# Kernel optimization log

Hardware: AMD Instinct MI355X
Metric: run time of the kernel (lower is better)

The kernel has to match this reference:

```python
import jax, jax.numpy as jnp
import numpy as np

N, E, B, D = 50000, 800000, 250, 128
EPS = 1e-5


def setup_inputs() -> dict:
    key = jax.random.key(0)
    ks = jax.random.split(key, 12)
    x = jax.random.normal(ks[0], (N, D), jnp.float32)
    w = jax.random.uniform(ks[1], (E, 4), jnp.float32)
    src = jax.random.randint(ks[2], (E,), 0, N)
    dst = jax.random.randint(ks[3], (E,), 0, N)
    graph_ids = jnp.sort(jax.random.randint(ks[4], (N,), 0, B))
    s = 1.0 / np.sqrt(D)
    W1 = jax.random.normal(ks[5], (D, D), jnp.float32) * s
    W2 = jax.random.normal(ks[6], (D, D), jnp.float32) * s
    W3 = jax.random.normal(ks[7], (D, D), jnp.float32) * s
    ln1_g = jnp.ones((D,), jnp.float32)
    ln1_b = jnp.zeros((D,), jnp.float32)
    ln2_g = jnp.ones((D,), jnp.float32)
    ln2_b = jnp.zeros((D,), jnp.float32)
    return dict(x=x, w=w, W1=W1, W2=W2, W3=W3, ln1_g=ln1_g, ln1_b=ln1_b,
                ln2_g=ln2_g, ln2_b=ln2_b, src=src, dst=dst, graph_ids=graph_ids)


def _layernorm(h, g, b):
    mu = jnp.mean(h, axis=-1, keepdims=True)
    var = jnp.mean(jnp.square(h - mu), axis=-1, keepdims=True)
    return (h - mu) * jax.lax.rsqrt(var + EPS) * g + b


def reference(x, w, W1, W2, W3, ln1_g, ln1_b, ln2_g, ln2_b, src, dst, graph_ids):
    # edge feature [E,Fe] -> scalar edge weight [E] (mean over feature dim)
    w_s = jnp.mean(w, axis=-1)
    ones_e = jnp.ones((E,), x.dtype)
    # DGL norm='both': unweighted degrees, clamped to >= 1
    out_deg = jnp.clip(jax.ops.segment_sum(ones_e, src, num_segments=N), 1.0)
    in_deg = jnp.clip(jax.ops.segment_sum(ones_e, dst, num_segments=N), 1.0)
    out_norm = jax.lax.rsqrt(out_deg)[:, None]  # [N,1]
    in_norm = jax.lax.rsqrt(in_deg)[:, None]    # [N,1]

    def gconv(h, W):
        m = (h * out_norm)[src] * w_s[:, None]                 # [E,D] gather-mul
        agg = jax.ops.segment_sum(m, dst, num_segments=N)      # [N,D] scatter-add
        return (agg * in_norm) @ W                              # [N,D_out]

    h = _layernorm(jax.nn.relu(gconv(x, W1)), ln1_g, ln1_b)
    h = _layernorm(jax.nn.relu(gconv(h, W2)), ln2_g, ln2_b)
    h = gconv(h, W3)
    # per-graph segmented sum readout -> [B, D]
    return jax.ops.segment_sum(h, graph_ids, num_segments=B)
```

## Files before the change

kernel.cpp:

```cpp
#include <hip/hip_runtime.h>

#define D 128
#define RS 16
#define NBMAX 1024
constexpr float EPS = 1e-5f;

typedef short bf16x8 __attribute__((ext_vector_type(8)));
typedef float f32x4 __attribute__((ext_vector_type(4)));
typedef unsigned long long u64;

__device__ __forceinline__ uint f2bf(float f) {
  union { float f; uint u; } v; v.f = f;
  return (v.u + 0x7fffu + ((v.u >> 16) & 1u)) >> 16;
}
__device__ __forceinline__ float bflo(uint u) {
  union { uint u; float f; } v; v.u = u << 16; return v.f;
}
__device__ __forceinline__ float bfhi(uint u) {
  union { uint u; float f; } v; v.u = u & 0xffff0000u; return v.f;
}

__device__ __forceinline__ int lower_bound(const int* __restrict__ a, int n, int key) {
  int lo = 0, hi = n;
  while (lo < hi) { int m = (lo + hi) >> 1; if (a[m] < key) lo = m + 1; else hi = m; }
  return lo;
}

__global__ __launch_bounds__(256) void k_pre(
    const int* __restrict__ src, const int* __restrict__ dst,
    int* __restrict__ ocnt, int* __restrict__ btot, int E, int nb, int ebA,
    const float4* __restrict__ x, uint4* __restrict__ xb, int n8, int cb,
    const float* __restrict__ W1, const float* __restrict__ W2,
    const float* __restrict__ W3, ushort* __restrict__ Wf) {
  __shared__ int hloc[NBMAX];
  int bid = blockIdx.x;
  int tid = threadIdx.x;
  if (bid < ebA) {
    for (int j = tid; j < nb; j += 256) hloc[j] = 0;
    __syncthreads();
    int e0 = bid * 4096;
#pragma unroll 4
    for (int it = 0; it < 16; ++it) {
      int e = e0 + it * 256 + tid;
      if (e < E) {
        atomicAdd(&ocnt[src[e]], 1);
        atomicAdd(&hloc[dst[e] >> 6], 1);
      }
    }
    __syncthreads();
    for (int j = tid; j < nb; j += 256) {
      int c = hloc[j];
      if (c) atomicAdd(&btot[j], c);
    }
  } else if (bid < ebA + cb) {
    int i = (bid - ebA) * 256 + tid;
    if (i < n8) {
      float4 p = x[i * 2], q = x[i * 2 + 1];
      uint4 o;
      o.x = f2bf(p.x) | (f2bf(p.y) << 16);
      o.y = f2bf(p.z) | (f2bf(p.w) << 16);
      o.z = f2bf(q.x) | (f2bf(q.y) << 16);
      o.w = f2bf(q.z) | (f2bf(q.w) << 16);
      xb[i] = o;
    }
  } else {
    int t4 = (bid - ebA - cb) * 256 + tid;
    if (t4 < 3 * 2048) {
      const float* Wsrc = (t4 < 2048) ? W1 : (t4 < 4096) ? W2 : W3;
      int t = t4 & 2047;
      int lane = t & 63;
      int frag = t >> 6;
      int ks = frag >> 3, ct = frag & 7;
      int col = ct * 16 + (lane & 15);
      int kb = ks * 32 + (lane >> 4) * 8;
      uint p[8];
#pragma unroll
      for (int j = 0; j < 8; ++j) p[j] = f2bf(Wsrc[(kb + j) * D + col]);
      uint4 o;
      o.x = p[0] | (p[1] << 16);
      o.y = p[2] | (p[3] << 16);
      o.z = p[4] | (p[5] << 16);
      o.w = p[6] | (p[7] << 16);
      *(uint4*)(Wf + (size_t)t4 * 8) = o;
    }
  }
}

__global__ void k_onorm(const int* __restrict__ ocnt, float* __restrict__ outn, int N) {
  int n = blockIdx.x * 256 + threadIdx.x;
  if (n < N) outn[n] = rsqrtf(fmaxf((float)ocnt[n], 1.0f));
}

__global__ __launch_bounds__(1024) void k_bbase(const int* __restrict__ btot,
                                                int* __restrict__ bb,
                                                int* __restrict__ rowptr,
                                                int nb, int E, int N) {
  __shared__ int part[1024];
  int t = threadIdx.x;
  int v = (t < nb) ? btot[t] : 0;
  part[t] = v;
  __syncthreads();
  for (int off = 1; off < 1024; off <<= 1) {
    int u = (t >= off) ? part[t - off] : 0;
    __syncthreads();
    part[t] += u;
    __syncthreads();
  }
  if (t < nb) bb[t] = part[t] - v;
  if (t == 0) { bb[nb] = E; rowptr[N] = E; }
}

__global__ __launch_bounds__(256) void k_bscatter(
    const int* __restrict__ src, const int* __restrict__ dst,
    const float4* __restrict__ w, const float* __restrict__ outn,
    const int* __restrict__ bb, int* __restrict__ bcur,
    u64* __restrict__ ebuf, int E, int nb) {
  __shared__ int hloc[NBMAX];
  __shared__ int hcur[NBMAX];
  int bid = blockIdx.x, tid = threadIdx.x;
  for (int j = tid; j < nb; j += 256) hloc[j] = 0;
  __syncthreads();
  int e0 = bid * 4096;
#pragma unroll 4
  for (int it = 0; it < 16; ++it) {
    int e = e0 + it * 256 + tid;
    if (e < E) atomicAdd(&hloc[dst[e] >> 6], 1);
  }
  __syncthreads();
  for (int j = tid; j < nb; j += 256) {
    int c = hloc[j];
    hcur[j] = c ? (bb[j] + atomicAdd(&bcur[j], c)) : 0;
  }
  __syncthreads();
#pragma unroll 4
  for (int it = 0; it < 16; ++it) {
    int e = e0 + it * 256 + tid;
    if (e < E) {
      int d = dst[e], s = src[e];
      int pos = atomicAdd(&hcur[d >> 6], 1);
      float4 wv = w[e];
      float coef = (wv.x + wv.y + wv.z + wv.w) * 0.25f * outn[s];
      u64 pk = ((u64)__float_as_uint(coef) << 32) |
               ((u64)(d & 63) << 16) | (uint)s;
      ebuf[pos] = pk;
    }
  }
}

__global__ __launch_bounds__(256) void k_bplace(
    const u64* __restrict__ ebuf, const int* __restrict__ bb,
    int* __restrict__ rowptr, float* __restrict__ innm,
    u64* __restrict__ ecsr, int N) {
  __shared__ int c64[64], ex[64], cur[64];
  int b = blockIdx.x, tid = threadIdx.x;
  int base = bb[b];
  int cnt = bb[b + 1] - base;
  if (tid < 64) c64[tid] = 0;
  __syncthreads();
  for (int i = tid; i < cnt; i += 256) {
    u64 v = ebuf[base + i];
    atomicAdd(&c64[(int)((v >> 16) & 63)], 1);
  }
  __syncthreads();
  if (tid < 64) {
    int cv = c64[tid];
    int inc = cv;
#pragma unroll
    for (int off = 1; off < 64; off <<= 1) {
      int u = __shfl_up(inc, off);
      if (tid >= off) inc += u;
    }
    int excl = inc - cv;
    ex[tid] = excl;
    cur[tid] = 0;
    int node = b * 64 + tid;
    if (node < N) {
      rowptr[node] = base + excl;
      innm[node] = rsqrtf(fmaxf((float)cv, 1.0f));
    }
  }
  __syncthreads();
  for (int i = tid; i < cnt; i += 256) {
    u64 v = ebuf[base + i];
    int dl = (int)((v >> 16) & 63);
    int pos = base + ex[dl] + atomicAdd(&cur[dl], 1);
    ecsr[pos] = (v & 0xFFFFFFFF00000000ull) | (v & 0xFFFFull);
  }
}

__global__ __launch_bounds__(128) void k_fused(
    const ushort* __restrict__ h, const int* __restrict__ rowptr,
    const u64* __restrict__ ecsr,
    const float* __restrict__ innm, const ushort* __restrict__ Wf,
    const float* __restrict__ g, const float* __restrict__ bta,
    void* __restrict__ out, int N, int do_ln) {
  __shared__ float lds[16 * D];
  const int lane = threadIdx.x & 63;
  const int wid = threadIdx.x >> 6;
  const int lr = lane & 15, lg = lane >> 4;
  const int row0 = blockIdx.x * 16;
  const int row = row0 + lr;
  const bool valid = row < N;

  int beg = 0, end = 0;
  float sc = 0.f;
  if (valid) { beg = rowptr[row]; end = rowptr[row + 1]; sc = innm[row]; }

  float a0[8], a1[8], a2[8], a3[8];
#pragma unroll
  for (int i = 0; i < 8; ++i) { a0[i] = 0; a1[i] = 0; a2[i] = 0; a3[i] = 0; }

#define EDGE(J)                                                  \
  {                                                              \
    u64 v = ecsr[J];                                             \
    float cf = __uint_as_float((uint)(v >> 32));                 \
    int s = (int)(v & 0xFFFFFFFFu);                              \
    const ushort* hp = h + (size_t)s * D + lg * 8;               \
    uint4 q0 = *(const uint4*)(hp);                              \
    uint4 q1 = *(const uint4*)(hp + 32);                         \
    uint4 q2 = *(const uint4*)(hp + 64);                         \
    uint4 q3 = *(const uint4*)(hp + 96);                         \
    a0[0] = fmaf(bflo(q0.x), cf, a0[0]); a0[1] = fmaf(bfhi(q0.x), cf, a0[1]); \
    a0[2] = fmaf(bflo(q0.y), cf, a0[2]); a0[3] = fmaf(bfhi(q0.y), cf, a0[3]); \
    a0[4] = fmaf(bflo(q0.z), cf, a0[4]); a0[5] = fmaf(bfhi(q0.z), cf, a0[5]); \
    a0[6] = fmaf(bflo(q0.w), cf, a0[6]); a0[7] = fmaf(bfhi(q0.w), cf, a0[7]); \
    a1[0] = fmaf(bflo(q1.x), cf, a1[0]); a1[1] = fmaf(bfhi(q1.x), cf, a1[1]); \
    a1[2] = fmaf(bflo(q1.y), cf, a1[2]); a1[3] = fmaf(bfhi(q1.y), cf, a1[3]); \
    a1[4] = fmaf(bflo(q1.z), cf, a1[4]); a1[5] = fmaf(bfhi(q1.z), cf, a1[5]); \
    a1[6] = fmaf(bflo(q1.w), cf, a1[6]); a1[7] = fmaf(bfhi(q1.w), cf, a1[7]); \
    a2[0] = fmaf(bflo(q2.x), cf, a2[0]); a2[1] = fmaf(bfhi(q2.x), cf, a2[1]); \
    a2[2] = fmaf(bflo(q2.y), cf, a2[2]); a2[3] = fmaf(bfhi(q2.y), cf, a2[3]); \
    a2[4] = fmaf(bflo(q2.z), cf, a2[4]); a2[5] = fmaf(bfhi(q2.z), cf, a2[5]); \
    a2[6] = fmaf(bflo(q2.w), cf, a2[6]); a2[7] = fmaf(bfhi(q2.w), cf, a2[7]); \
    a3[0] = fmaf(bflo(q3.x), cf, a3[0]); a3[1] = fmaf(bfhi(q3.x), cf, a3[1]); \
    a3[2] = fmaf(bflo(q3.y), cf, a3[2]); a3[3] = fmaf(bfhi(q3.y), cf, a3[3]); \
    a3[4] = fmaf(bflo(q3.z), cf, a3[4]); a3[5] = fmaf(bfhi(q3.z), cf, a3[5]); \
    a3[6] = fmaf(bflo(q3.w), cf, a3[6]); a3[7] = fmaf(bfhi(q3.w), cf, a3[7]); \
  }

  int j = beg + wid;
  for (; j + 2 < end; j += 4) { EDGE(j) EDGE(j + 2) }
  if (j < end) EDGE(j)
#undef EDGE

  if (wid == 1) {
#pragma unroll
    for (int i = 0; i < 8; ++i) {
      lds[i * 64 + lane]        = a0[i];
      lds[(i + 8) * 64 + lane]  = a1[i];
      lds[(i + 16) * 64 + lane] = a2[i];
      lds[(i + 24) * 64 + lane] = a3[i];
    }
  }
  __syncthreads();
  if (wid == 1) return;
#pragma unroll
  for (int i = 0; i < 8; ++i) {
    a0[i] += lds[i * 64 + lane];
    a1[i] += lds[(i + 8) * 64 + lane];
    a2[i] += lds[(i + 16) * 64 + lane];
    a3[i] += lds[(i + 24) * 64 + lane];
  }
  asm volatile("s_waitcnt lgkmcnt(0)" ::: "memory");
  __builtin_amdgcn_sched_barrier(0);

  uint4 fa[4];
#define PACK(dst, A)                                             \
  dst.x = f2bf(A[0] * sc) | (f2bf(A[1] * sc) << 16);             \
  dst.y = f2bf(A[2] * sc) | (f2bf(A[3] * sc) << 16);             \
  dst.z = f2bf(A[4] * sc) | (f2bf(A[5] * sc) << 16);             \
  dst.w = f2bf(A[6] * sc) | (f2bf(A[7] * sc) << 16);
  PACK(fa[0], a0) PACK(fa[1], a1) PACK(fa[2], a2) PACK(fa[3], a3)
#undef PACK

  f32x4 acc[8];
#pragma unroll
  for (int ct = 0; ct < 8; ++ct) acc[ct] = (f32x4){0.f, 0.f, 0.f, 0.f};
#pragma unroll
  for (int ks = 0; ks < 4; ++ks) {
    bf16x8 av;
    __builtin_memcpy(&av, &fa[ks], 16);
    const ushort* wp = Wf + ((size_t)(ks * 8) * 64 + lane) * 8;
#pragma unroll
    for (int ct = 0; ct < 8; ++ct) {
      bf16x8 b = *(const bf16x8*)(wp + ct * 512);
      acc[ct] = __builtin_amdgcn_mfma_f32_16x16x32_bf16(av, b, acc[ct], 0, 0, 0);
    }
  }

  if (do_ln) {
    float v[8][4];
#pragma unroll
    for (int ct = 0; ct < 8; ++ct)
#pragma unroll
      for (int j2 = 0; j2 < 4; ++j2) v[ct][j2] = fmaxf(acc[ct][j2], 0.f);
    float mu[4], rs[4];
#pragma unroll
    for (int j2 = 0; j2 < 4; ++j2) {
      float s = 0.f;
#pragma unroll
      for (int ct = 0; ct < 8; ++ct) s += v[ct][j2];
#pragma unroll
      for (int off = 1; off < 16; off <<= 1) s += __shfl_xor(s, off);
      mu[j2] = s * (1.0f / D);
    }
#pragma unroll
    for (int j2 = 0; j2 < 4; ++j2) {
      float q = 0.f;
#pragma unroll
      for (int ct = 0; ct < 8; ++ct) {
        v[ct][j2] -= mu[j2];
        q = fmaf(v[ct][j2], v[ct][j2], q);
      }
#pragma unroll
      for (int off = 1; off < 16; off <<= 1) q += __shfl_xor(q, off);
      rs[j2] = rsqrtf(q * (1.0f / D) + EPS);
    }
    ushort* lp = (ushort*)&lds[0];
#pragma unroll
    for (int ct = 0; ct < 8; ++ct) {
      float gc = g[ct * 16 + lr], bc = bta[ct * 16 + lr];
#pragma unroll
      for (int j2 = 0; j2 < 4; ++j2)
        lp[(lg * 4 + j2) * D + ct * 16 + lr] = (ushort)f2bf(fmaf(v[ct][j2] * rs[j2], gc, bc));
    }
    __builtin_amdgcn_wave_barrier();
    int r = row0 + (lane >> 2);
    if (r < N) {
      ushort* ob = (ushort*)out + (size_t)row0 * D + lane * 32;
#pragma unroll
      for (int i = 0; i < 4; ++i)
        ((uint4*)ob)[i] = ((const uint4*)(lp + lane * 32))[i];
    }
  } else {
    float* lp = &lds[0];
#pragma unroll
    for (int ct = 0; ct < 8; ++ct)
#pragma unroll
      for (int j2 = 0; j2 < 4; ++j2)
        lp[(lg * 4 + j2) * D + ct * 16 + lr] = acc[ct][j2];
    __builtin_amdgcn_wave_barrier();
    int r = row0 + (lane >> 2);
    if (r < N) {
      float* ob = (float*)out + (size_t)row0 * D + lane * 32;
#pragma unroll
      for (int i = 0; i < 8; ++i)
        ((float4*)ob)[i] = ((const float4*)(lp + lane * 32))[i];
    }
  }
}

__global__ __launch_bounds__(128) void k_rpart(
    const float* __restrict__ h, const int* __restrict__ gid,
    float* __restrict__ part, int N) {
  int b = blockIdx.x / RS, s = blockIdx.x % RS;
  int t = threadIdx.x;
  int start = lower_bound(gid, N, b);
  int end = lower_bound(gid, N, b + 1);
  int len = end - start;
  int chunk = (len + RS - 1) / RS;
  int rb = start + s * chunk;
  int re = min(rb + chunk, end);
  float acc = 0.f;
  for (int n = rb; n < re; ++n) acc += h[(size_t)n * D + t];
  part[((size_t)b * RS + s) * D + t] = acc;
}

__global__ __launch_bounds__(128) void k_rsum(
    const float* __restrict__ part, float* __restrict__ out) {
  int b = blockIdx.x;
  int t = threadIdx.x;
  float acc = 0.f;
#pragma unroll
  for (int s = 0; s < RS; ++s) acc += part[((size_t)b * RS + s) * D + t];
  out[(size_t)b * D + t] = acc;
}

extern "C" void kernel_launch(void* const* d_in, const int* in_sizes, int n_in,
                              void* d_out, int out_size, void* d_ws, size_t ws_size,
                              hipStream_t stream) {
  const float* x    = (const float*)d_in[0];
  const float* w    = (const float*)d_in[1];
  const float* W1   = (const float*)d_in[2];
  const float* W2   = (const float*)d_in[3];
  const float* W3   = (const float*)d_in[4];
  const float* ln1g = (const float*)d_in[5];
  const float* ln1b = (const float*)d_in[6];
  const float* ln2g = (const float*)d_in[7];
  const float* ln2b = (const float*)d_in[8];
  const int* src = (const int*)d_in[9];
  const int* dst = (const int*)d_in[10];
  const int* gid = (const int*)d_in[11];
  const int N = in_sizes[0] / D;
  const int E = in_sizes[9];
  const int B = out_size / D;
  float* outp = (float*)d_out;

  float*  h3f  = (float*)d_ws;
  ushort* xb   = (ushort*)(h3f + (size_t)N * D);
  ushort* hb1  = xb + (size_t)N * D;
  ushort* Wf   = hb1 + (size_t)N * D;
  float*  outn = (float*)(Wf + 3 * 2048 * 8);
  float*  innm = outn + N;
  const int nb  = (N + 63) >> 6;
  const int ebA = (E + 4095) / 4096;
  int*    ocnt = (int*)(innm + N);
  int*    btot = ocnt + N;
  int*    bcur = btot + nb;
  int*    rowptr = bcur + nb;
  int*    bb   = rowptr + N + 2;
  u64*    ecsr = (u64*)(bb + nb + 2);
  float*  part = (float*)(ecsr + E);
  u64*    ebuf = (u64*)h3f;

  const int mb  = (N + 15) / 16;
  const int n8  = N * D / 8;
  const int cb  = (n8 + 255) / 256;

  hipMemsetAsync(ocnt, 0, sizeof(int) * ((size_t)N + 2 * nb), stream);
  k_pre<<<ebA + cb + 24, 256, 0, stream>>>(src, dst, ocnt, btot, E, nb, ebA,
                                           (const float4*)x, (uint4*)xb, n8, cb,
                                           W1, W2, W3, Wf);
  k_onorm<<<(N + 255) / 256, 256, 0, stream>>>(ocnt, outn, N);
  k_bbase<<<1, 1024, 0, stream>>>(btot, bb, rowptr, nb, E, N);
  k_bscatter<<<ebA, 256, 0, stream>>>(src, dst, (const float4*)w, outn, bb, bcur,
                                      ebuf, E, nb);
  k_bplace<<<nb, 256, 0, stream>>>(ebuf, bb, rowptr, innm, ecsr, N);

  k_fused<<<mb, 128, 0, stream>>>(xb, rowptr, ecsr, innm, Wf,
                                  ln1g, ln1b, hb1, N, 1);
  k_fused<<<mb, 128, 0, stream>>>(hb1, rowptr, ecsr, innm, Wf + 16384,
                                  ln2g, ln2b, xb, N, 1);
  k_fused<<<mb, 128, 0, stream>>>(xb, rowptr, ecsr, innm, Wf + 32768,
                                  nullptr, nullptr, h3f, N, 0);

  k_rpart<<<B * RS, 128, 0, stream>>>(h3f, gid, part, N);
  k_rsum<<<B, 128, 0, stream>>>(part, outp);
}
```

Baseline: 238.7 us.

## Sub-sort CSR edges by source chunk and use nontemporal loads/stores

The CSR placement kernel now buckets each destination row's edges by source-node chunk (src>>13, 8 chunks), using a 512-bin block-wide scan. Edges within a row are therefore ordered by source region, which should make the gathers of h across the fused kernel's row-parallel lanes hit nearby memory and improve L2 locality. Edge-list loads and output stores also become nontemporal so streamed data does not evict h from cache. The cost is a heavier scan in the placement kernel, with many syncthreads.

```diff
diff --git a/kernel.cpp b/kernel.cpp
--- a/kernel.cpp
+++ b/kernel.cpp
@@ -3,10 +3,13 @@
 #define D 128
 #define RS 16
 #define NBMAX 1024
+#define CSH 13
+#define NCH 8
 constexpr float EPS = 1e-5f;
 
 typedef short bf16x8 __attribute__((ext_vector_type(8)));
 typedef float f32x4 __attribute__((ext_vector_type(4)));
+typedef uint u32x4 __attribute__((ext_vector_type(4)));
 typedef unsigned long long u64;
 
 __device__ __forceinline__ uint f2bf(float f) {
@@ -151,39 +154,50 @@
     const u64* __restrict__ ebuf, const int* __restrict__ bb,
     int* __restrict__ rowptr, float* __restrict__ innm,
     u64* __restrict__ ecsr, int N) {
-  __shared__ int c64[64], ex[64], cur[64];
+  __shared__ int cnt[64 * NCH], ex[64 * NCH], cur[64 * NCH], psum[256];
   int b = blockIdx.x, tid = threadIdx.x;
   int base = bb[b];
-  int cnt = bb[b + 1] - base;
-  if (tid < 64) c64[tid] = 0;
-  __syncthreads();
-  for (int i = tid; i < cnt; i += 256) {
+  int tote = bb[b + 1] - base;
+  cnt[2 * tid] = 0; cnt[2 * tid + 1] = 0;
+  __syncthreads();
+  for (int i = tid; i < tote; i += 256) {
     u64 v = ebuf[base + i];
-    atomicAdd(&c64[(int)((v >> 16) & 63)], 1);
-  }
-  __syncthreads();
+    int dl = (int)((v >> 16) & 63);
+    int c = (int)((v & 0xFFFFu) >> CSH);
+    atomicAdd(&cnt[dl * NCH + c], 1);
+  }
+  __syncthreads();
+  int p = cnt[2 * tid] + cnt[2 * tid + 1];
+  psum[tid] = p;
+  __syncthreads();
+  for (int off = 1; off < 256; off <<= 1) {
+    int u = (tid >= off) ? psum[tid - off] : 0;
+    __syncthreads();
+    psum[tid] += u;
+    __syncthreads();
+  }
+  int excl = psum[tid] - p;
+  ex[2 * tid] = excl;
+  ex[2 * tid + 1] = excl + cnt[2 * tid];
+  cur[2 * tid] = 0; cur[2 * tid + 1] = 0;
+  __syncthreads();
+  int total = psum[255];
   if (tid < 64) {
-    int cv = c64[tid];
-    int inc = cv;
-#pragma unroll
-    for (int off = 1; off < 64; off <<= 1) {
-      int u = __shfl_up(inc, off);
-      if (tid >= off) inc += u;
-    }
-    int excl = inc - cv;
-    ex[tid] = excl;
-    cur[tid] = 0;
     int node = b * 64 + tid;
     if (node < N) {
-      rowptr[node] = base + excl;
-      innm[node] = rsqrtf(fmaxf((float)cv, 1.0f));
-    }
-  }
-  __syncthreads();
-  for (int i = tid; i < cnt; i += 256) {
+      int st = ex[tid * NCH];
+      int en = (tid < 63) ? ex[(tid + 1) * NCH] : total;
+      rowptr[node] = base + st;
+      innm[node] = rsqrtf(fmaxf((float)(en - st), 1.0f));
+    }
+  }
+  __syncthreads();
+  for (int i = tid; i < tote; i += 256) {
     u64 v = ebuf[base + i];
     int dl = (int)((v >> 16) & 63);
-    int pos = base + ex[dl] + atomicAdd(&cur[dl], 1);
+    int c = (int)((v & 0xFFFFu) >> CSH);
+    int slot = dl * NCH + c;
+    int pos = base + ex[slot] + atomicAdd(&cur[slot], 1);
     ecsr[pos] = (v & 0xFFFFFFFF00000000ull) | (v & 0xFFFFull);
   }
 }
@@ -212,7 +226,7 @@
 
 #define EDGE(J)                                                  \
   {                                                              \
-    u64 v = ecsr[J];                                             \
+    u64 v = __builtin_nontemporal_load(&ecsr[J]);                \
     float cf = __uint_as_float((uint)(v >> 32));                 \
     int s = (int)(v & 0xFFFFFFFFu);                              \
     const ushort* hp = h + (size_t)s * D + lg * 8;               \
@@ -330,7 +344,7 @@
       ushort* ob = (ushort*)out + (size_t)row0 * D + lane * 32;
 #pragma unroll
       for (int i = 0; i < 4; ++i)
-        ((uint4*)ob)[i] = ((const uint4*)(lp + lane * 32))[i];
+        __builtin_nontemporal_store(((const u32x4*)(lp + lane * 32))[i], (u32x4*)ob + i);
     }
   } else {
     float* lp = &lds[0];
@@ -345,7 +359,7 @@
       float* ob = (float*)out + (size_t)row0 * D + lane * 32;
 #pragma unroll
       for (int i = 0; i < 8; ++i)
-        ((float4*)ob)[i] = ((const float4*)(lp + lane * 32))[i];
+        __builtin_nontemporal_store(((const f32x4*)(lp + lane * 32))[i], (f32x4*)ob + i);
     }
   }
 }
```

After: 266.1 us. +11.5%, slower.
